# Optimization experiments

Measured on AMD Instinct MI355X. Metric: run time of the kernel, lower is better.

## Reference

```python
import jax, jax.numpy as jnp
import numpy as np

N_OBS = 8_000_000
N_PTS = 1_000_000
N_CAMS = 2_000


def setup_inputs() -> dict:
    key = jax.random.key(0)
    k1, k2, k3, k4, k5 = jax.random.split(key, 5)
    points_2d = jax.random.normal(k1, (N_OBS, 2), dtype=jnp.float32) * 100.0
    pose = jax.random.normal(k2, (N_CAMS, 7), dtype=jnp.float32)
    points_3d = jax.random.normal(k3, (N_PTS, 3), dtype=jnp.float32)
    camera_indices = jax.random.randint(k4, (N_OBS,), 0, N_CAMS, dtype=jnp.int64)
    point_indices = jax.random.randint(k5, (N_OBS,), 0, N_PTS, dtype=jnp.int64)
    # pinhole intrinsics: fx=fy=1000, cx=cy=500
    K = jnp.array([[1000.0, 0.0, 500.0],
                   [0.0, 1000.0, 500.0],
                   [0.0, 0.0, 1.0]], dtype=jnp.float32)
    return {"points_2d": points_2d, "K": K, "pose": pose,
            "points_3d": points_3d, "camera_indices": camera_indices,
            "point_indices": point_indices}


def rotate_quat(points, cam7):
    # cam7[:, :4] = quaternion (w, x, y, z), cam7[:, 4:7] = translation
    q = cam7[:, :4]
    q = q / jnp.linalg.norm(q, axis=-1, keepdims=True)
    w, qv = q[:, :1], q[:, 1:]            # [N,1], [N,3]
    uv = 2.0 * jnp.cross(qv, points)      # [N,3]
    rotated = points + w * uv + jnp.cross(qv, uv)
    return rotated + cam7[:, 4:7]


def homo2cart(p):
    return p[:, :2] / p[:, 2:3]


def reference(points_2d, K, pose, points_3d, camera_indices, point_indices):
    pts = points_3d[point_indices]        # gather [N_OBS,3]
    cam = pose[camera_indices]            # gather [N_OBS,7]
    points_proj = rotate_quat(pts, cam)
    pixels = points_proj @ K.T            # [N_OBS,3]
    pixels = homo2cart(pixels)            # [N_OBS,2]
    return pixels - points_2d
```

## Files before the change

kernel.cpp:

```cpp
#include <hip/hip_runtime.h>


typedef int   i32x4 __attribute__((ext_vector_type(4)));
typedef float f32x4 __attribute__((ext_vector_type(4)));
typedef float f32x4a __attribute__((ext_vector_type(4), aligned(4)));
typedef int   i32x2 __attribute__((ext_vector_type(2)));

__global__ void prep_pose(const float* __restrict__ pose,
                          float* __restrict__ pose8, int nCams)
{
    int r = blockIdx.x * blockDim.x + threadIdx.x;
    if (r >= nCams) return;
    const float* src = pose + 7 * r;
    float qw = src[0], qx = src[1], qy = src[2], qz = src[3];
    float inv = 1.0f / sqrtf(qw*qw + qx*qx + qy*qy + qz*qz);
    f32x4 q; q.x = qw*inv; q.y = qx*inv; q.z = qy*inv; q.w = qz*inv;
    f32x4 t; t.x = src[4]; t.y = src[5]; t.z = src[6]; t.w = 0.0f;
    *(f32x4*)(pose8 + 8*r)     = q;
    *(f32x4*)(pose8 + 8*r + 4) = t;
}

__global__ void prep_pts(const float* __restrict__ pts3,
                         float* __restrict__ pts4, int nPts)
{
    int r = blockIdx.x * blockDim.x + threadIdx.x;
    if (r >= nPts) return;
    f32x4 v;
    v.x = pts3[3*r]; v.y = pts3[3*r + 1]; v.z = pts3[3*r + 2]; v.w = 0.0f;
    *(f32x4*)(pts4 + 4*r) = v;
}

__global__ void __launch_bounds__(256, 8)
reproj_main(const f32x4* __restrict__ p2d,
            const float* __restrict__ K,
            const f32x4* __restrict__ pose8,
            const f32x4* __restrict__ pts4,
            const i32x4* __restrict__ camIdx,
            const i32x4* __restrict__ ptIdx,
            f32x4*       __restrict__ out,
            int nQuads)
{
    int i = blockIdx.x * blockDim.x + threadIdx.x;
    if (i >= nQuads) return;

    i32x4 ci = __builtin_nontemporal_load(&camIdx[i]);
    i32x4 pi = __builtin_nontemporal_load(&ptIdx[i]);
    f32x4 pA = __builtin_nontemporal_load(&p2d[2*i]);
    f32x4 pB = __builtin_nontemporal_load(&p2d[2*i + 1]);

    float K00 = K[0], K01 = K[1], K02 = K[2];
    float K10 = K[3], K11 = K[4], K12 = K[5];
    float K20 = K[6], K21 = K[7], K22 = K[8];

    auto project = [&](int c, int pidx, float& ox, float& oy) {
        f32x4 q4 = pose8[2*c];
        f32x4 t4 = pose8[2*c + 1];
        f32x4 v  = pts4[pidx];
        float qw = q4.x, qx = q4.y, qy = q4.z, qz = q4.w;
        float x = v.x, y = v.y, z = v.z;

        float uvx = 2.0f * (qy*z - qz*y);
        float uvy = 2.0f * (qz*x - qx*z);
        float uvz = 2.0f * (qx*y - qy*x);

        float rx = x + qw*uvx + (qy*uvz - qz*uvy) + t4.x;
        float ry = y + qw*uvy + (qz*uvx - qx*uvz) + t4.y;
        float rz = z + qw*uvz + (qx*uvy - qy*uvx) + t4.z;

        float px = K00*rx + K01*ry + K02*rz;
        float py = K10*rx + K11*ry + K12*rz;
        float pz = K20*rx + K21*ry + K22*rz;

        ox = px / pz;
        oy = py / pz;
    };

    float x0,y0,x1,y1,x2,y2,x3,y3;
    project(ci.x, pi.x, x0, y0);
    project(ci.y, pi.y, x1, y1);
    project(ci.z, pi.z, x2, y2);
    project(ci.w, pi.w, x3, y3);

    f32x4 rA, rB;
    rA.x = x0 - pA.x; rA.y = y0 - pA.y; rA.z = x1 - pA.z; rA.w = y1 - pA.w;
    rB.x = x2 - pB.x; rB.y = y2 - pB.y; rB.z = x3 - pB.z; rB.w = y3 - pB.w;
    __builtin_nontemporal_store(rA, &out[2*i]);
    __builtin_nontemporal_store(rB, &out[2*i + 1]);
}

__global__ void __launch_bounds__(256, 8)
reproj_fallback(const f32x4* __restrict__ p2d,
                const float* __restrict__ K,
                const float* __restrict__ pose,
                const float* __restrict__ pts3d,
                const i32x2* __restrict__ camIdx,
                const i32x2* __restrict__ ptIdx,
                f32x4*       __restrict__ out,
                int nPairs, int nPts)
{
    int i = blockIdx.x * blockDim.x + threadIdx.x;
    if (i >= nPairs) return;

    i32x2 ci = __builtin_nontemporal_load(&camIdx[i]);
    i32x2 pi = __builtin_nontemporal_load(&ptIdx[i]);
    f32x4 p  = __builtin_nontemporal_load(&p2d[i]);

    float K00 = K[0], K01 = K[1], K02 = K[2];
    float K10 = K[3], K11 = K[4], K12 = K[5];
    float K20 = K[6], K21 = K[7], K22 = K[8];

    auto project = [&](int c, int pidx, float& ox, float& oy) {
        f32x4 q4 = *(const f32x4a*)(pose + 7*c);
        f32x4 t4 = *(const f32x4a*)(pose + 7*c + 3);
        float qw = q4.x, qx = q4.y, qy = q4.z, qz = q4.w;
        float tx = t4.y, ty = t4.z, tz = t4.w;

        float inv = 1.0f / sqrtf(qw*qw + qx*qx + qy*qy + qz*qz);
        qw *= inv; qx *= inv; qy *= inv; qz *= inv;

        float x, y, z;
        if (pidx < nPts - 1) {
            f32x4 v = *(const f32x4a*)(pts3d + 3*pidx);
            x = v.x; y = v.y; z = v.z;
        } else {
            f32x4 v = *(const f32x4a*)(pts3d + 3*pidx - 1);
            x = v.y; y = v.z; z = v.w;
        }

        float uvx = 2.0f * (qy*z - qz*y);
        float uvy = 2.0f * (qz*x - qx*z);
        float uvz = 2.0f * (qx*y - qy*x);

        float rx = x + qw*uvx + (qy*uvz - qz*uvy) + tx;
        float ry = y + qw*uvy + (qz*uvx - qx*uvz) + ty;
        float rz = z + qw*uvz + (qx*uvy - qy*uvx) + tz;

        float px = K00*rx + K01*ry + K02*rz;
        float py = K10*rx + K11*ry + K12*rz;
        float pz = K20*rx + K21*ry + K22*rz;

        ox = px / pz;
        oy = py / pz;
    };

    float ax, ay, bx, by;
    project(ci.x, pi.x, ax, ay);
    project(ci.y, pi.y, bx, by);

    f32x4 r;
    r.x = ax - p.x; r.y = ay - p.y; r.z = bx - p.z; r.w = by - p.w;
    __builtin_nontemporal_store(r, &out[i]);
}

extern "C" void kernel_launch(void* const* d_in, const int* in_sizes, int n_in,
                              void* d_out, int out_size, void* d_ws, size_t ws_size,
                              hipStream_t stream)
{
    const float* points_2d = (const float*)d_in[0];
    const float* K         = (const float*)d_in[1];
    const float* pose      = (const float*)d_in[2];
    const float* points_3d = (const float*)d_in[3];
    const int*   camIdx    = (const int*)d_in[4];
    const int*   ptIdx    = (const int*)d_in[5];
    float*       out       = (float*)d_out;

    int nObs  = in_sizes[4];
    int nCams = in_sizes[2] / 7;
    int nPts  = in_sizes[3] / 3;

    size_t poseBytes = (size_t)nCams * 8 * sizeof(float);
    size_t ptsOff    = 65536;
    size_t needed    = ptsOff + (size_t)nPts * 4 * sizeof(float);

    const int block = 256;

    if (ws_size >= needed && nObs % 4 == 0 && poseBytes <= ptsOff) {
        float* pose8 = (float*)d_ws;
        float* pts4  = (float*)((char*)d_ws + ptsOff);

        prep_pose<<<(nCams + block - 1) / block, block, 0, stream>>>(pose, pose8, nCams);
        prep_pts<<<(nPts + block - 1) / block, block, 0, stream>>>(points_3d, pts4, nPts);

        int nQuads = nObs / 4;
        int grid = (nQuads + block - 1) / block;
        reproj_main<<<grid, block, 0, stream>>>(
            (const f32x4*)points_2d, K, (const f32x4*)pose8, (const f32x4*)pts4,
            (const i32x4*)camIdx, (const i32x4*)ptIdx,
            (f32x4*)out, nQuads);
    } else {
        int nPairs = nObs / 2;
        int grid = (nPairs + block - 1) / block;
        reproj_fallback<<<grid, block, 0, stream>>>(
            (const f32x4*)points_2d, K, pose, points_3d,
            (const i32x2*)camIdx, (const i32x2*)ptIdx,
            (f32x4*)out, nPairs, nPts);
    }
}
```

Baseline: 295.0 us.

## Drop padded points prep pass and gather 3D points directly

Removes the prep_pts kernel that copied the 1M points into a padded float4 workspace, and has the main kernel gather xyz directly from the packed 3-float array using unaligned 16-byte loads, with a bounds-safe path for the last point. The main kernel also drops from four to two observations per thread. This saves a 12MB read plus 16MB write pass and one launch. In exchange, gathers may be misaligned and straddle cache lines more often, and each thread carries less work.

```diff
diff --git a/kernel.cpp b/kernel.cpp
--- a/kernel.cpp
+++ b/kernel.cpp
@@ -1,10 +1,9 @@
 #include <hip/hip_runtime.h>
 
 
-typedef int   i32x4 __attribute__((ext_vector_type(4)));
+typedef int   i32x2 __attribute__((ext_vector_type(2)));
 typedef float f32x4 __attribute__((ext_vector_type(4)));
 typedef float f32x4a __attribute__((ext_vector_type(4), aligned(4)));
-typedef int   i32x2 __attribute__((ext_vector_type(2)));
 
 __global__ void prep_pose(const float* __restrict__ pose,
                           float* __restrict__ pose8, int nCams)
@@ -20,33 +19,22 @@
     *(f32x4*)(pose8 + 8*r + 4) = t;
 }
 
-__global__ void prep_pts(const float* __restrict__ pts3,
-                         float* __restrict__ pts4, int nPts)
-{
-    int r = blockIdx.x * blockDim.x + threadIdx.x;
-    if (r >= nPts) return;
-    f32x4 v;
-    v.x = pts3[3*r]; v.y = pts3[3*r + 1]; v.z = pts3[3*r + 2]; v.w = 0.0f;
-    *(f32x4*)(pts4 + 4*r) = v;
-}
-
 __global__ void __launch_bounds__(256, 8)
 reproj_main(const f32x4* __restrict__ p2d,
             const float* __restrict__ K,
             const f32x4* __restrict__ pose8,
-            const f32x4* __restrict__ pts4,
-            const i32x4* __restrict__ camIdx,
-            const i32x4* __restrict__ ptIdx,
+            const float* __restrict__ pts3d,
+            const i32x2* __restrict__ camIdx,
+            const i32x2* __restrict__ ptIdx,
             f32x4*       __restrict__ out,
-            int nQuads)
+            int nPairs, int nPts)
 {
     int i = blockIdx.x * blockDim.x + threadIdx.x;
-    if (i >= nQuads) return;
+    if (i >= nPairs) return;
 
-    i32x4 ci = __builtin_nontemporal_load(&camIdx[i]);
-    i32x4 pi = __builtin_nontemporal_load(&ptIdx[i]);
-    f32x4 pA = __builtin_nontemporal_load(&p2d[2*i]);
-    f32x4 pB = __builtin_nontemporal_load(&p2d[2*i + 1]);
+    i32x2 ci = __builtin_nontemporal_load(&camIdx[i]);
+    i32x2 pi = __builtin_nontemporal_load(&ptIdx[i]);
+    f32x4 p  = __builtin_nontemporal_load(&p2d[i]);
 
     float K00 = K[0], K01 = K[1], K02 = K[2];
     float K10 = K[3], K11 = K[4], K12 = K[5];
@@ -55,9 +43,16 @@
     auto project = [&](int c, int pidx, float& ox, float& oy) {
         f32x4 q4 = pose8[2*c];
         f32x4 t4 = pose8[2*c + 1];
-        f32x4 v  = pts4[pidx];
         float qw = q4.x, qx = q4.y, qy = q4.z, qz = q4.w;
-        float x = v.x, y = v.y, z = v.z;
+
+        float x, y, z;
+        if (pidx < nPts - 1) {
+            f32x4 v = *(const f32x4a*)(pts3d + 3*pidx);
+            x = v.x; y = v.y; z = v.z;
+        } else {
+            f32x4 v = *(const f32x4a*)(pts3d + 3*pidx - 1);
+            x = v.y; y = v.z; z = v.w;
+        }
 
         float uvx = 2.0f * (qy*z - qz*y);
         float uvy = 2.0f * (qz*x - qx*z);
@@ -75,17 +70,13 @@
         oy = py / pz;
     };
 
-    float x0,y0,x1,y1,x2,y2,x3,y3;
-    project(ci.x, pi.x, x0, y0);
-    project(ci.y, pi.y, x1, y1);
-    project(ci.z, pi.z, x2, y2);
-    project(ci.w, pi.w, x3, y3);
+    float ax, ay, bx, by;
+    project(ci.x, pi.x, ax, ay);
+    project(ci.y, pi.y, bx, by);
 
-    f32x4 rA, rB;
-    rA.x = x0 - pA.x; rA.y = y0 - pA.y; rA.z = x1 - pA.z; rA.w = y1 - pA.w;
-    rB.x = x2 - pB.x; rB.y = y2 - pB.y; rB.z = x3 - pB.z; rB.w = y3 - pB.w;
-    __builtin_nontemporal_store(rA, &out[2*i]);
-    __builtin_nontemporal_store(rB, &out[2*i + 1]);
+    f32x4 r;
+    r.x = ax - p.x; r.y = ay - p.y; r.z = bx - p.z; r.w = by - p.w;
+    __builtin_nontemporal_store(r, &out[i]);
 }
 
 __global__ void __launch_bounds__(256, 8)
@@ -161,35 +152,27 @@
     const float* pose      = (const float*)d_in[2];
     const float* points_3d = (const float*)d_in[3];
     const int*   camIdx    = (const int*)d_in[4];
-    const int*   ptIdx    = (const int*)d_in[5];
+    const int*   ptIdx     = (const int*)d_in[5];
     float*       out       = (float*)d_out;
 
     int nObs  = in_sizes[4];
     int nCams = in_sizes[2] / 7;
     int nPts  = in_sizes[3] / 3;
+    int nPairs = nObs / 2;
 
     size_t poseBytes = (size_t)nCams * 8 * sizeof(float);
-    size_t ptsOff    = 65536;
-    size_t needed    = ptsOff + (size_t)nPts * 4 * sizeof(float);
 
     const int block = 256;
+    int grid = (nPairs + block - 1) / block;
 
-    if (ws_size >= needed && nObs % 4 == 0 && poseBytes <= ptsOff) {
+    if (ws_size >= poseBytes && nObs % 2 == 0) {
         float* pose8 = (float*)d_ws;
-        float* pts4  = (float*)((char*)d_ws + ptsOff);
-
         prep_pose<<<(nCams + block - 1) / block, block, 0, stream>>>(pose, pose8, nCams);
-        prep_pts<<<(nPts + block - 1) / block, block, 0, stream>>>(points_3d, pts4, nPts);
-
-        int nQuads = nObs / 4;
-        int grid = (nQuads + block - 1) / block;
         reproj_main<<<grid, block, 0, stream>>>(
-            (const f32x4*)points_2d, K, (const f32x4*)pose8, (const f32x4*)pts4,
-            (const i32x4*)camIdx, (const i32x4*)ptIdx,
-            (f32x4*)out, nQuads);
+            (const f32x4*)points_2d, K, (const f32x4*)pose8, points_3d,
+            (const i32x2*)camIdx, (const i32x2*)ptIdx,
+            (f32x4*)out, nPairs, nPts);
     } else {
-        int nPairs = nObs / 2;
-        int grid = (nPairs + block - 1) / block;
         reproj_fallback<<<grid, block, 0, stream>>>(
             (const f32x4*)points_2d, K, pose, points_3d,
             (const i32x2*)camIdx, (const i32x2*)ptIdx,
```

Result: faster. 267.8 us (-9.2%).
